# Optimization experiments

Measured on AMD Instinct MI355X. Metric: run time of the kernel, lower is better.

Reference implementation:

```python
import jax, jax.numpy as jnp
import numpy as np

N_USER, N_ITEM = 100000, 50000
D, H, B, E = 64, 64, 16384, 2000000

def _xavier(key, shape):
    fan_in, fan_out = shape[0], shape[1]
    lim = float(np.sqrt(6.0 / (fan_in + fan_out)))
    return jax.random.uniform(key, shape, jnp.float32, -lim, lim)

def setup_inputs() -> dict:
    key = jax.random.key(0)
    ks = jax.random.split(key, 16)
    inp = {
        "user_table": _xavier(ks[0], (N_USER, D)),
        "item_table": _xavier(ks[1], (N_ITEM, D)),
        "Wu": _xavier(ks[2], (D, D)),   # GCN_user weight ([in,out])
        "bu": jnp.zeros((D,), jnp.float32),
        "Wi": _xavier(ks[3], (D, D)),   # GCN_item weight
        "bi": jnp.zeros((D,), jnp.float32),
        "W1": _xavier(ks[4], (4 * D, 2 * H)),
        "b1": jnp.zeros((2 * H,), jnp.float32),
        "W2": _xavier(ks[5], (2 * H, H)),
        "b2": jnp.zeros((H,), jnp.float32),
        "W3": _xavier(ks[6], (H, 1)),
        "b3": jnp.zeros((1,), jnp.float32),
        "user_bias": jnp.zeros((N_USER, 1), jnp.float32),
        "item_bias": jnp.zeros((N_ITEM, 1), jnp.float32),
        "user_id": jax.random.randint(ks[7], (B,), 0, N_USER),
        "item_id": jax.random.randint(ks[8], (B,), 0, N_ITEM),
        "edge_user": jax.random.randint(ks[9], (E,), 0, N_USER),
        "edge_item": jax.random.randint(ks[10], (E,), 0, N_ITEM),
    }
    return inp

def reference(user_table, item_table, Wu, bu, Wi, bi, W1, b1, W2, b2, W3, b3,
              user_bias, item_bias, user_id, item_id, edge_user, edge_item):
    # sparse.mm(edge_ui, item_h)[user_id]: aggregate item embeddings per user
    agg_i = jax.ops.segment_sum(item_table[edge_item], edge_user, num_segments=N_USER)[user_id]
    agg_u = jax.ops.segment_sum(user_table[edge_user], edge_item, num_segments=N_ITEM)[item_id]
    ones_e = jnp.ones((edge_user.shape[0],), jnp.float32)
    deg_u = jax.ops.segment_sum(ones_e, edge_user, num_segments=N_USER)[user_id] + 1.0  # item_din
    deg_i = jax.ops.segment_sum(ones_e, edge_item, num_segments=N_ITEM)[item_id] + 1.0  # user_din
    gcn_item_h = agg_i / deg_u[:, None]   # [B, D]
    gcn_user_h = agg_u / deg_i[:, None]   # [B, D]
    # dropout p=0.3 is identity in eval mode
    gcn_user_out = jax.nn.relu(gcn_user_h @ Wu + bu)
    gcn_item_out = jax.nn.relu(gcn_item_h @ Wi + bi)
    u_emb = user_table[user_id]
    i_emb = item_table[item_id]
    x = jnp.concatenate([u_emb * i_emb,
                         u_emb * gcn_item_out,
                         gcn_user_out * i_emb,
                         gcn_user_out * gcn_item_out], axis=-1)  # [B, 4D]
    x1 = jnp.tanh(x @ W1 + b1)
    x2 = jnp.tanh(x1 @ W2 + b2)
    x3 = (x2 @ W3 + b3).reshape(-1)
    return x3 + user_bias[user_id, 0] + item_bias[item_id, 0]
```

## Files before the change

### kernel.cpp

```cpp
#include <hip/hip_runtime.h>
#include <cstdint>
#include <cstddef>

#define D 64
#define CAPU 96
#define CAPI 128
#define OCAP 4096

__global__ __launch_bounds__(256) void k_build_maps(const int* __restrict__ user_id,
                                                    const int* __restrict__ item_id,
                                                    int* __restrict__ map_u,
                                                    int* __restrict__ map_i, int B)
{
    int i = blockIdx.x * blockDim.x + threadIdx.x;
    if (i < B) {
        atomicCAS(&map_u[user_id[i]], -1, i);
        atomicCAS(&map_i[item_id[i]], -1, i);
    }
}

__global__ __launch_bounds__(256) void k_scatter(const int* __restrict__ edge_user,
                                                 const int* __restrict__ edge_item,
                                                 const int* __restrict__ map_u,
                                                 const int* __restrict__ map_i,
                                                 int* __restrict__ cntU,
                                                 int* __restrict__ cntI,
                                                 uint32_t* __restrict__ listU,
                                                 uint32_t* __restrict__ listI,
                                                 int* __restrict__ ovfCnt,
                                                 uint32_t* __restrict__ ovf, int E)
{
    int t = blockIdx.x * blockDim.x + threadIdx.x;
    int base = t * 4;
    if (base >= E) return;

    int us[4], is[4];
    int cnt4 = 4;
    if (base + 3 < E) {
        int4 eu = *(const int4*)(edge_user + base);
        int4 ei = *(const int4*)(edge_item + base);
        us[0] = eu.x; us[1] = eu.y; us[2] = eu.z; us[3] = eu.w;
        is[0] = ei.x; is[1] = ei.y; is[2] = ei.z; is[3] = ei.w;
    } else {
        cnt4 = E - base;
        for (int q = 0; q < cnt4; ++q) { us[q] = edge_user[base + q]; is[q] = edge_item[base + q]; }
    }

    #pragma unroll
    for (int q = 0; q < 4; ++q) {
        if (q >= cnt4) break;
        int u = us[q], it = is[q];
        int su = map_u[u];
        int si = map_i[it];
        if (su >= 0) {
            int pos = atomicAdd(&cntU[su * 16], 1);
            if (pos < CAPU) listU[(size_t)su * CAPU + pos] = (uint32_t)it;
            else { int o = atomicAdd(ovfCnt, 1);
                   if (o < OCAP) ovf[o] = ((uint32_t)su << 17) | (uint32_t)it; }
        }
        if (si >= 0) {
            int pos = atomicAdd(&cntI[si * 16], 1);
            if (pos < CAPI) listI[(size_t)si * CAPI + pos] = (uint32_t)u;
            else { int o = atomicAdd(ovfCnt, 1);
                   if (o < OCAP) ovf[o] = 0x80000000u | ((uint32_t)si << 17) | (uint32_t)u; }
        }
    }
}

__global__ __launch_bounds__(256) void k_gather(const uint32_t* __restrict__ listU,
                                                const uint32_t* __restrict__ listI,
                                                const int* __restrict__ cntU,
                                                const int* __restrict__ cntI,
                                                const float* __restrict__ user_table,
                                                const float* __restrict__ item_table,
                                                const int* __restrict__ ovfCnt,
                                                const uint32_t* __restrict__ ovf,
                                                float* __restrict__ aggIU,
                                                float* __restrict__ aggUI,
                                                int* __restrict__ degU,
                                                int* __restrict__ degI, int B)
{
    int gg = (blockIdx.x * blockDim.x + threadIdx.x) >> 4;
    if (gg >= 2 * B) return;
    int l16 = threadIdx.x & 15;
    int side = gg >= B;
    int slot = side ? gg - B : gg;

    int cnt = side ? cntI[slot * 16] : cntU[slot * 16];
    int caps = side ? CAPI : CAPU;
    int n = cnt < caps ? cnt : caps;
    const uint32_t* list = side ? (listI + (size_t)slot * CAPI)
                                : (listU + (size_t)slot * CAPU);
    const float4* table4 = (const float4*)(side ? user_table : item_table);

    float4 a0 = {0.f, 0.f, 0.f, 0.f};
    float4 a1 = {0.f, 0.f, 0.f, 0.f};
    int j = 0;
    #pragma unroll 2
    for (; j + 2 <= n; j += 2) {
        int r0 = (int)list[j];
        int r1 = (int)list[j + 1];
        float4 v0 = table4[(size_t)r0 * 16 + l16];
        float4 v1 = table4[(size_t)r1 * 16 + l16];
        a0.x += v0.x; a0.y += v0.y; a0.z += v0.z; a0.w += v0.w;
        a1.x += v1.x; a1.y += v1.y; a1.z += v1.z; a1.w += v1.w;
    }
    if (j < n) {
        int r0 = (int)list[j];
        float4 v0 = table4[(size_t)r0 * 16 + l16];
        a0.x += v0.x; a0.y += v0.y; a0.z += v0.z; a0.w += v0.w;
    }
    if (cnt > caps) {
        int on = *ovfCnt; if (on > OCAP) on = OCAP;
        for (int k = 0; k < on; ++k) {
            uint32_t p = ovf[k];
            if ((int)(p >> 31) == side && (int)((p >> 17) & 0x3FFFu) == slot) {
                float4 v = table4[(size_t)(p & 0x1FFFFu) * 16 + l16];
                a0.x += v.x; a0.y += v.y; a0.z += v.z; a0.w += v.w;
            }
        }
    }
    float4 acc = {a0.x + a1.x, a0.y + a1.y, a0.z + a1.z, a0.w + a1.w};
    float4* agg4 = (float4*)(side ? aggUI : aggIU);
    agg4[(size_t)slot * 16 + l16] = acc;
    if (l16 == 0) (side ? degI : degU)[slot] = cnt;
}

__global__ __launch_bounds__(1024) void k_build_x(const int* __restrict__ user_id,
                                                  const int* __restrict__ item_id,
                                                  const int* __restrict__ map_u,
                                                  const int* __restrict__ map_i,
                                                  const int* __restrict__ degU,
                                                  const int* __restrict__ degI,
                                                  const float* __restrict__ aggIU,
                                                  const float* __restrict__ aggUI,
                                                  const float* __restrict__ user_table,
                                                  const float* __restrict__ item_table,
                                                  const float* __restrict__ Wu,
                                                  const float* __restrict__ bu,
                                                  const float* __restrict__ Wi,
                                                  const float* __restrict__ bi,
                                                  float* __restrict__ x, int B)
{
    __shared__ float WuL[D * D];
    __shared__ float WiL[D * D];
    for (int t = threadIdx.x; t < D * D; t += blockDim.x) {
        WuL[t] = Wu[t];
        WiL[t] = Wi[t];
    }
    __syncthreads();

    int wid = (blockIdx.x * blockDim.x + threadIdx.x) >> 6;
    int lane = threadIdx.x & 63;
    if (wid >= B) return;

    int u  = user_id[wid];
    int it = item_id[wid];
    int su = map_u[u];
    int si = map_i[it];
    float du = (float)degU[su] + 1.0f;
    float di = (float)degI[si] + 1.0f;
    float gih = aggIU[(size_t)su * D + lane] / du;
    float guh = aggUI[(size_t)si * D + lane] / di;

    float accU = bu[lane];
    float accI = bi[lane];
    #pragma unroll 8
    for (int k = 0; k < D; ++k) {
        float gk = __shfl(guh, k);
        accU = fmaf(gk, WuL[k * D + lane], accU);
        float hk = __shfl(gih, k);
        accI = fmaf(hk, WiL[k * D + lane], accI);
    }
    float guo = fmaxf(accU, 0.0f);
    float gio = fmaxf(accI, 0.0f);
    float ue = user_table[(size_t)u * D + lane];
    float ie = item_table[(size_t)it * D + lane];

    size_t xb = (size_t)wid * 256;
    x[xb + lane]       = ue * ie;
    x[xb + 64 + lane]  = ue * gio;
    x[xb + 128 + lane] = guo * ie;
    x[xb + 192 + lane] = guo * gio;
}

__global__ __launch_bounds__(256) void k_gemm1(const float* __restrict__ x,
                                               const float* __restrict__ W1,
                                               const float* __restrict__ b1,
                                               float* __restrict__ x1, int B)
{
    __shared__ float xs[32][65];
    __shared__ float ws[32][128];
    int tid = threadIdx.x;
    int tx = tid & 31;
    int ty = tid >> 5;
    int row0 = blockIdx.x * 64;
    float acc[8][4] = {};

    for (int k0 = 0; k0 < 256; k0 += 32) {
        {
            int r = tid >> 2;
            int kk = (tid & 3) * 8;
            const float4* src = (const float4*)&x[(size_t)(row0 + r) * 256 + k0 + kk];
            float4 v0 = src[0], v1 = src[1];
            xs[kk + 0][r] = v0.x; xs[kk + 1][r] = v0.y; xs[kk + 2][r] = v0.z; xs[kk + 3][r] = v0.w;
            xs[kk + 4][r] = v1.x; xs[kk + 5][r] = v1.y; xs[kk + 6][r] = v1.z; xs[kk + 7][r] = v1.w;
        }
        {
            const float4* src = (const float4*)(W1 + (size_t)k0 * 128);
            float4* dst = (float4*)&ws[0][0];
            #pragma unroll
            for (int q = 0; q < 4; ++q) dst[tid + q * 256] = src[tid + q * 256];
        }
        __syncthreads();
        #pragma unroll
        for (int k = 0; k < 32; ++k) {
            float a[8], b[4];
            #pragma unroll
            for (int r = 0; r < 8; ++r) a[r] = xs[k][ty * 8 + r];
            #pragma unroll
            for (int c = 0; c < 4; ++c) b[c] = ws[k][tx + 32 * c];
            #pragma unroll
            for (int r = 0; r < 8; ++r)
                #pragma unroll
                for (int c = 0; c < 4; ++c)
                    acc[r][c] = fmaf(a[r], b[c], acc[r][c]);
        }
        __syncthreads();
    }
    #pragma unroll
    for (int r = 0; r < 8; ++r) {
        int row = row0 + ty * 8 + r;
        #pragma unroll
        for (int c = 0; c < 4; ++c) {
            int col = tx + 32 * c;
            x1[(size_t)row * 128 + col] = tanhf(acc[r][c] + b1[col]);
        }
    }
}

__global__ __launch_bounds__(256) void k_gemm2f(const float* __restrict__ x1,
                                                const float* __restrict__ W2,
                                                const float* __restrict__ b2,
                                                const float* __restrict__ W3,
                                                const float* __restrict__ b3,
                                                const float* __restrict__ user_bias,
                                                const float* __restrict__ item_bias,
                                                const int* __restrict__ user_id,
                                                const int* __restrict__ item_id,
                                                float* __restrict__ out, int B)
{
    __shared__ float xs[32][65];
    __shared__ float ws[32][64];
    int tid = threadIdx.x;
    int tx = tid & 15;
    int ty = tid >> 4;
    int row0 = blockIdx.x * 64;
    float acc[4][4] = {};

    for (int k0 = 0; k0 < 128; k0 += 32) {
        {
            int r = tid >> 2;
            int kk = (tid & 3) * 8;
            const float4* src = (const float4*)&x1[(size_t)(row0 + r) * 128 + k0 + kk];
            float4 v0 = src[0], v1 = src[1];
            xs[kk + 0][r] = v0.x; xs[kk + 1][r] = v0.y; xs[kk + 2][r] = v0.z; xs[kk + 3][r] = v0.w;
            xs[kk + 4][r] = v1.x; xs[kk + 5][r] = v1.y; xs[kk + 6][r] = v1.z; xs[kk + 7][r] = v1.w;
        }
        {
            const float4* src = (const float4*)(W2 + (size_t)k0 * 64);
            float4* dst = (float4*)&ws[0][0];
            #pragma unroll
            for (int q = 0; q < 2; ++q) dst[tid + q * 256] = src[tid + q * 256];
        }
        __syncthreads();
        #pragma unroll
        for (int k = 0; k < 32; ++k) {
            float a[4], b[4];
            #pragma unroll
            for (int r = 0; r < 4; ++r) a[r] = xs[k][ty * 4 + r];
            #pragma unroll
            for (int c = 0; c < 4; ++c) b[c] = ws[k][tx + 16 * c];
            #pragma unroll
            for (int r = 0; r < 4; ++r)
                #pragma unroll
                for (int c = 0; c < 4; ++c)
                    acc[r][c] = fmaf(a[r], b[c], acc[r][c]);
        }
        __syncthreads();
    }

    float w3v[4], b2v[4];
    #pragma unroll
    for (int c = 0; c < 4; ++c) {
        int col = tx + 16 * c;
        w3v[c] = W3[col];
        b2v[c] = b2[col];
    }
    #pragma unroll
    for (int r = 0; r < 4; ++r) {
        float p = 0.f;
        #pragma unroll
        for (int c = 0; c < 4; ++c)
            p += tanhf(acc[r][c] + b2v[c]) * w3v[c];
        p += __shfl_xor(p, 1);
        p += __shfl_xor(p, 2);
        p += __shfl_xor(p, 4);
        p += __shfl_xor(p, 8);
        if (tx == 0) {
            int row = row0 + ty * 4 + r;
            out[row] = p + b3[0] + user_bias[user_id[row]] + item_bias[item_id[row]];
        }
    }
}

extern "C" void kernel_launch(void* const* d_in, const int* in_sizes, int n_in,
                              void* d_out, int out_size, void* d_ws, size_t ws_size,
                              hipStream_t stream)
{
    const float* user_table = (const float*)d_in[0];
    const float* item_table = (const float*)d_in[1];
    const float* Wu = (const float*)d_in[2];
    const float* bu = (const float*)d_in[3];
    const float* Wi = (const float*)d_in[4];
    const float* bi = (const float*)d_in[5];
    const float* W1 = (const float*)d_in[6];
    const float* b1 = (const float*)d_in[7];
    const float* W2 = (const float*)d_in[8];
    const float* b2 = (const float*)d_in[9];
    const float* W3 = (const float*)d_in[10];
    const float* b3 = (const float*)d_in[11];
    const float* user_bias = (const float*)d_in[12];
    const float* item_bias = (const float*)d_in[13];
    const int* user_id = (const int*)d_in[14];
    const int* item_id = (const int*)d_in[15];
    const int* edge_user = (const int*)d_in[16];
    const int* edge_item = (const int*)d_in[17];

    const int N_USER = in_sizes[0] / D;
    const int N_ITEM = in_sizes[1] / D;
    const int B = in_sizes[14];
    const int E = in_sizes[16];

    char* ws = (char*)d_ws;
    const size_t aggIU_off = 0;
    const size_t aggUI_off = aggIU_off + (size_t)B * D * 4;
    const size_t degU_off  = aggUI_off + (size_t)B * D * 4;
    const size_t degI_off  = degU_off + (size_t)B * 4;
    const size_t mapu_off  = degI_off + (size_t)B * 4;
    const size_t mapi_off  = mapu_off + (size_t)N_USER * 4;
    size_t x_off = mapi_off + (size_t)N_ITEM * 4;
    x_off = (x_off + 255) & ~(size_t)255;
    const size_t x1_off = x_off + (size_t)B * 256 * 4;

    float* aggIU = (float*)(ws + aggIU_off);
    float* aggUI = (float*)(ws + aggUI_off);
    int*   degU  = (int*)(ws + degU_off);
    int*   degI  = (int*)(ws + degI_off);
    int*   map_u = (int*)(ws + mapu_off);
    int*   map_i = (int*)(ws + mapi_off);
    float* x  = (float*)(ws + x_off);
    float* x1 = (float*)(ws + x1_off);

    uint32_t* listU = (uint32_t*)(ws + x_off);
    uint32_t* listI = listU + (size_t)B * CAPU;
    int* cntU = (int*)(ws + x1_off);
    int* cntI = cntU + (size_t)B * 16;
    int* ovfCnt = cntI + (size_t)B * 16;
    uint32_t* ovf = (uint32_t*)(ovfCnt + 64);

    hipMemsetAsync(ws + mapu_off, 0xFF, (size_t)(N_USER + N_ITEM) * 4, stream);
    hipMemsetAsync(cntU, 0, (size_t)B * 16 * 4 * 2 + 256 + OCAP * 4, stream);

    k_build_maps<<<(B + 255) / 256, 256, 0, stream>>>(user_id, item_id, map_u, map_i, B);

    k_scatter<<<(E / 4 + 255) / 256, 256, 0, stream>>>(edge_user, edge_item, map_u, map_i,
                                                       cntU, cntI, listU, listI, ovfCnt, ovf, E);

    k_gather<<<(2 * B) / 16, 256, 0, stream>>>(listU, listI, cntU, cntI,
                                               user_table, item_table, ovfCnt, ovf,
                                               aggIU, aggUI, degU, degI, B);

    k_build_x<<<B / 16, 1024, 0, stream>>>(user_id, item_id, map_u, map_i, degU, degI,
                                           aggIU, aggUI, user_table, item_table,
                                           Wu, bu, Wi, bi, x, B);

    k_gemm1<<<B / 64, 256, 0, stream>>>(x, W1, b1, x1, B);

    k_gemm2f<<<B / 64, 256, 0, stream>>>(x1, W2, b2, W3, b3, user_bias, item_bias,
                                         user_id, item_id, (float*)d_out, B);
}
```

Baseline: 272.7 us.

## Fuse feature construction with MLP layers and tile GCN linear layers

The degree normalization moves into the gather kernel. The per-row shuffle GCN matmul is replaced by a tiled 32-row GEMM kernel that writes GCN outputs. The separate x-build, GEMM1 and GEMM2 kernels are merged into one MLP kernel that builds the elementwise products on the fly in shared memory, so the 16 MB x tensor and the x1 intermediate no longer round-trip through global memory. The cost is a heavier kernel with about 50 KB of shared memory, smaller 32-row tiles (fewer reuses of W1 per load), and the embedding rows being re-gathered per chunk.

```diff
diff --git a/kernel.cpp b/kernel.cpp
--- a/kernel.cpp
+++ b/kernel.cpp
@@ -6,6 +6,7 @@
 #define CAPU 96
 #define CAPI 128
 #define OCAP 4096
+#define GR 32
 
 __global__ __launch_bounds__(256) void k_build_maps(const int* __restrict__ user_id,
                                                     const int* __restrict__ item_id,
@@ -76,9 +77,7 @@
                                                 const int* __restrict__ ovfCnt,
                                                 const uint32_t* __restrict__ ovf,
                                                 float* __restrict__ aggIU,
-                                                float* __restrict__ aggUI,
-                                                int* __restrict__ degU,
-                                                int* __restrict__ degI, int B)
+                                                float* __restrict__ aggUI, int B)
 {
     int gg = (blockIdx.x * blockDim.x + threadIdx.x) >> 4;
     if (gg >= 2 * B) return;
@@ -120,197 +119,195 @@
             }
         }
     }
-    float4 acc = {a0.x + a1.x, a0.y + a1.y, a0.z + a1.z, a0.w + a1.w};
+    float inv = 1.0f / ((float)cnt + 1.0f);
+    float4 acc = {(a0.x + a1.x) * inv, (a0.y + a1.y) * inv,
+                  (a0.z + a1.z) * inv, (a0.w + a1.w) * inv};
     float4* agg4 = (float4*)(side ? aggUI : aggIU);
     agg4[(size_t)slot * 16 + l16] = acc;
-    if (l16 == 0) (side ? degI : degU)[slot] = cnt;
-}
-
-__global__ __launch_bounds__(1024) void k_build_x(const int* __restrict__ user_id,
-                                                  const int* __restrict__ item_id,
-                                                  const int* __restrict__ map_u,
-                                                  const int* __restrict__ map_i,
-                                                  const int* __restrict__ degU,
-                                                  const int* __restrict__ degI,
-                                                  const float* __restrict__ aggIU,
-                                                  const float* __restrict__ aggUI,
-                                                  const float* __restrict__ user_table,
-                                                  const float* __restrict__ item_table,
-                                                  const float* __restrict__ Wu,
-                                                  const float* __restrict__ bu,
-                                                  const float* __restrict__ Wi,
-                                                  const float* __restrict__ bi,
-                                                  float* __restrict__ x, int B)
-{
-    __shared__ float WuL[D * D];
-    __shared__ float WiL[D * D];
-    for (int t = threadIdx.x; t < D * D; t += blockDim.x) {
-        WuL[t] = Wu[t];
-        WiL[t] = Wi[t];
+}
+
+__global__ __launch_bounds__(256) void k_gcn(const int* __restrict__ user_id,
+                                             const int* __restrict__ item_id,
+                                             const int* __restrict__ map_u,
+                                             const int* __restrict__ map_i,
+                                             const float* __restrict__ aggIU,
+                                             const float* __restrict__ aggUI,
+                                             const float* __restrict__ Wi,
+                                             const float* __restrict__ bi,
+                                             const float* __restrict__ Wu,
+                                             const float* __restrict__ bu,
+                                             float* __restrict__ Xgi,
+                                             float* __restrict__ Xgu, int B)
+{
+    __shared__ float A[GR][68];
+    __shared__ float Wl[64][64];
+    __shared__ int sslot[GR];
+    int t = threadIdx.x;
+    int nb = B / GR;
+    int b = blockIdx.x;
+    int side = b >= nb;
+    int row0 = (side ? b - nb : b) * GR;
+
+    if (t < GR) {
+        int r = row0 + t;
+        sslot[t] = side ? map_i[item_id[r]] : map_u[user_id[r]];
+    }
+    {
+        const float4* Wg = (const float4*)(side ? Wu : Wi);
+        float4* Wl4 = (float4*)&Wl[0][0];
+        #pragma unroll
+        for (int q = 0; q < 4; ++q) Wl4[t + q * 256] = Wg[t + q * 256];
     }
     __syncthreads();
-
-    int wid = (blockIdx.x * blockDim.x + threadIdx.x) >> 6;
-    int lane = threadIdx.x & 63;
-    if (wid >= B) return;
-
-    int u  = user_id[wid];
-    int it = item_id[wid];
-    int su = map_u[u];
-    int si = map_i[it];
-    float du = (float)degU[su] + 1.0f;
-    float di = (float)degI[si] + 1.0f;
-    float gih = aggIU[(size_t)su * D + lane] / du;
-    float guh = aggUI[(size_t)si * D + lane] / di;
-
-    float accU = bu[lane];
-    float accI = bi[lane];
-    #pragma unroll 8
-    for (int k = 0; k < D; ++k) {
-        float gk = __shfl(guh, k);
-        accU = fmaf(gk, WuL[k * D + lane], accU);
-        float hk = __shfl(gih, k);
-        accI = fmaf(hk, WiL[k * D + lane], accI);
-    }
-    float guo = fmaxf(accU, 0.0f);
-    float gio = fmaxf(accI, 0.0f);
-    float ue = user_table[(size_t)u * D + lane];
-    float ie = item_table[(size_t)it * D + lane];
-
-    size_t xb = (size_t)wid * 256;
-    x[xb + lane]       = ue * ie;
-    x[xb + 64 + lane]  = ue * gio;
-    x[xb + 128 + lane] = guo * ie;
-    x[xb + 192 + lane] = guo * gio;
-}
-
-__global__ __launch_bounds__(256) void k_gemm1(const float* __restrict__ x,
-                                               const float* __restrict__ W1,
-                                               const float* __restrict__ b1,
-                                               float* __restrict__ x1, int B)
-{
-    __shared__ float xs[32][65];
-    __shared__ float ws[32][128];
-    int tid = threadIdx.x;
-    int tx = tid & 31;
-    int ty = tid >> 5;
-    int row0 = blockIdx.x * 64;
-    float acc[8][4] = {};
-
-    for (int k0 = 0; k0 < 256; k0 += 32) {
+    {
+        const float4* agg4 = (const float4*)(side ? aggUI : aggIU);
+        #pragma unroll
+        for (int q = 0; q < 2; ++q) {
+            int idx = t * 2 + q;
+            int r = idx >> 4, l16 = idx & 15;
+            ((float4*)&A[r][0])[l16] = agg4[(size_t)sslot[r] * 16 + l16];
+        }
+    }
+    __syncthreads();
+
+    const float* bias = side ? bu : bi;
+    int tx = t & 15, ty = t >> 4;
+    float acc[2][4] = {};
+    for (int k = 0; k < 64; ++k) {
+        float a0 = A[2 * ty][k];
+        float a1 = A[2 * ty + 1][k];
+        #pragma unroll
+        for (int c = 0; c < 4; ++c) {
+            float w = Wl[k][tx + 16 * c];
+            acc[0][c] = fmaf(a0, w, acc[0][c]);
+            acc[1][c] = fmaf(a1, w, acc[1][c]);
+        }
+    }
+    float* Xg = side ? Xgu : Xgi;
+    #pragma unroll
+    for (int r = 0; r < 2; ++r) {
+        int row = row0 + 2 * ty + r;
+        #pragma unroll
+        for (int c = 0; c < 4; ++c) {
+            int col = tx + 16 * c;
+            Xg[(size_t)row * 64 + col] = fmaxf(acc[r][c] + bias[col], 0.f);
+        }
+    }
+}
+
+__global__ __launch_bounds__(256) void k_mlp(const int* __restrict__ user_id,
+                                             const int* __restrict__ item_id,
+                                             const float* __restrict__ user_table,
+                                             const float* __restrict__ item_table,
+                                             const float* __restrict__ Xgi,
+                                             const float* __restrict__ Xgu,
+                                             const float* __restrict__ W1,
+                                             const float* __restrict__ b1,
+                                             const float* __restrict__ W2,
+                                             const float* __restrict__ b2,
+                                             const float* __restrict__ W3,
+                                             const float* __restrict__ b3,
+                                             const float* __restrict__ user_bias,
+                                             const float* __restrict__ item_bias,
+                                             float* __restrict__ out, int B)
+{
+    __shared__ float Fbuf[64][68];
+    __shared__ float WB[8192];
+    __shared__ int sU[GR], sI[GR];
+    int t = threadIdx.x;
+    int row0 = blockIdx.x * GR;
+    if (t < GR) { sU[t] = user_id[row0 + t]; sI[t] = item_id[row0 + t]; }
+    __syncthreads();
+
+    int tx1 = t & 31, ty1 = t >> 5;
+    float acc1[4][4] = {};
+
+    const int fkA[4] = {0, 0, 3, 3};
+    const int fkB[4] = {1, 2, 1, 2};
+    for (int j = 0; j < 4; ++j) {
+        #pragma unroll
+        for (int half = 0; half < 2; ++half) {
+            int kind = half ? fkB[j] : fkA[j];
+            #pragma unroll
+            for (int q = 0; q < 2; ++q) {
+                int idx = t * 2 + q;
+                int r = idx >> 4, l16 = idx & 15;
+                const float4* src;
+                size_t rowidx;
+                if (kind == 0)      { src = (const float4*)user_table; rowidx = (size_t)sU[r]; }
+                else if (kind == 1) { src = (const float4*)item_table; rowidx = (size_t)sI[r]; }
+                else if (kind == 2) { src = (const float4*)Xgi; rowidx = (size_t)(row0 + r); }
+                else                { src = (const float4*)Xgu; rowidx = (size_t)(row0 + r); }
+                ((float4*)&Fbuf[half * 32 + r][0])[l16] = src[rowidx * 16 + l16];
+            }
+        }
         {
-            int r = tid >> 2;
-            int kk = (tid & 3) * 8;
-            const float4* src = (const float4*)&x[(size_t)(row0 + r) * 256 + k0 + kk];
-            float4 v0 = src[0], v1 = src[1];
-            xs[kk + 0][r] = v0.x; xs[kk + 1][r] = v0.y; xs[kk + 2][r] = v0.z; xs[kk + 3][r] = v0.w;
-            xs[kk + 4][r] = v1.x; xs[kk + 5][r] = v1.y; xs[kk + 6][r] = v1.z; xs[kk + 7][r] = v1.w;
-        }
-        {
-            const float4* src = (const float4*)(W1 + (size_t)k0 * 128);
-            float4* dst = (float4*)&ws[0][0];
-            #pragma unroll
-            for (int q = 0; q < 4; ++q) dst[tid + q * 256] = src[tid + q * 256];
+            const float4* w4 = (const float4*)W1 + (size_t)j * 2048;
+            float4* d = (float4*)WB;
+            #pragma unroll
+            for (int q = 0; q < 8; ++q) d[t + q * 256] = w4[t + q * 256];
         }
         __syncthreads();
-        #pragma unroll
-        for (int k = 0; k < 32; ++k) {
-            float a[8], b[4];
-            #pragma unroll
-            for (int r = 0; r < 8; ++r) a[r] = xs[k][ty * 8 + r];
-            #pragma unroll
-            for (int c = 0; c < 4; ++c) b[c] = ws[k][tx + 32 * c];
-            #pragma unroll
-            for (int r = 0; r < 8; ++r)
-                #pragma unroll
-                for (int c = 0; c < 4; ++c)
-                    acc[r][c] = fmaf(a[r], b[c], acc[r][c]);
-        }
-        __syncthreads();
-    }
-    #pragma unroll
-    for (int r = 0; r < 8; ++r) {
-        int row = row0 + ty * 8 + r;
-        #pragma unroll
-        for (int c = 0; c < 4; ++c) {
-            int col = tx + 32 * c;
-            x1[(size_t)row * 128 + col] = tanhf(acc[r][c] + b1[col]);
-        }
-    }
-}
-
-__global__ __launch_bounds__(256) void k_gemm2f(const float* __restrict__ x1,
-                                                const float* __restrict__ W2,
-                                                const float* __restrict__ b2,
-                                                const float* __restrict__ W3,
-                                                const float* __restrict__ b3,
-                                                const float* __restrict__ user_bias,
-                                                const float* __restrict__ item_bias,
-                                                const int* __restrict__ user_id,
-                                                const int* __restrict__ item_id,
-                                                float* __restrict__ out, int B)
-{
-    __shared__ float xs[32][65];
-    __shared__ float ws[32][64];
-    int tid = threadIdx.x;
-    int tx = tid & 15;
-    int ty = tid >> 4;
-    int row0 = blockIdx.x * 64;
-    float acc[4][4] = {};
-
-    for (int k0 = 0; k0 < 128; k0 += 32) {
-        {
-            int r = tid >> 2;
-            int kk = (tid & 3) * 8;
-            const float4* src = (const float4*)&x1[(size_t)(row0 + r) * 128 + k0 + kk];
-            float4 v0 = src[0], v1 = src[1];
-            xs[kk + 0][r] = v0.x; xs[kk + 1][r] = v0.y; xs[kk + 2][r] = v0.z; xs[kk + 3][r] = v0.w;
-            xs[kk + 4][r] = v1.x; xs[kk + 5][r] = v1.y; xs[kk + 6][r] = v1.z; xs[kk + 7][r] = v1.w;
-        }
-        {
-            const float4* src = (const float4*)(W2 + (size_t)k0 * 64);
-            float4* dst = (float4*)&ws[0][0];
-            #pragma unroll
-            for (int q = 0; q < 2; ++q) dst[tid + q * 256] = src[tid + q * 256];
-        }
-        __syncthreads();
-        #pragma unroll
-        for (int k = 0; k < 32; ++k) {
+        for (int k = 0; k < 64; ++k) {
             float a[4], b[4];
             #pragma unroll
-            for (int r = 0; r < 4; ++r) a[r] = xs[k][ty * 4 + r];
-            #pragma unroll
-            for (int c = 0; c < 4; ++c) b[c] = ws[k][tx + 16 * c];
+            for (int r = 0; r < 4; ++r)
+                a[r] = Fbuf[4 * ty1 + r][k] * Fbuf[32 + 4 * ty1 + r][k];
+            #pragma unroll
+            for (int c = 0; c < 4; ++c) b[c] = WB[k * 128 + tx1 + 32 * c];
             #pragma unroll
             for (int r = 0; r < 4; ++r)
                 #pragma unroll
                 for (int c = 0; c < 4; ++c)
-                    acc[r][c] = fmaf(a[r], b[c], acc[r][c]);
+                    acc1[r][c] = fmaf(a[r], b[c], acc1[r][c]);
         }
         __syncthreads();
     }
 
-    float w3v[4], b2v[4];
+    float* x1t = &Fbuf[0][0];
     #pragma unroll
-    for (int c = 0; c < 4; ++c) {
-        int col = tx + 16 * c;
-        w3v[c] = W3[col];
-        b2v[c] = b2[col];
-    }
+    for (int r = 0; r < 4; ++r)
+        #pragma unroll
+        for (int c = 0; c < 4; ++c) {
+            int col = tx1 + 32 * c;
+            x1t[(4 * ty1 + r) * 132 + col] = tanhf(acc1[r][c] + b1[col]);
+        }
+    {
+        const float4* w4 = (const float4*)W2;
+        float4* d = (float4*)WB;
+        #pragma unroll
+        for (int q = 0; q < 8; ++q) d[t + q * 256] = w4[t + q * 256];
+    }
+    __syncthreads();
+
+    int tx2 = t & 15, ty2 = t >> 4;
+    float acc2[2][4] = {};
+    for (int k = 0; k < 128; ++k) {
+        float a0 = x1t[(2 * ty2) * 132 + k];
+        float a1 = x1t[(2 * ty2 + 1) * 132 + k];
+        #pragma unroll
+        for (int c = 0; c < 4; ++c) {
+            float w = WB[k * 64 + tx2 + 16 * c];
+            acc2[0][c] = fmaf(a0, w, acc2[0][c]);
+            acc2[1][c] = fmaf(a1, w, acc2[1][c]);
+        }
+    }
+    float b3v = b3[0];
     #pragma unroll
-    for (int r = 0; r < 4; ++r) {
+    for (int r = 0; r < 2; ++r) {
+        int lr = 2 * ty2 + r;
         float p = 0.f;
         #pragma unroll
-        for (int c = 0; c < 4; ++c)
-            p += tanhf(acc[r][c] + b2v[c]) * w3v[c];
+        for (int c = 0; c < 4; ++c) {
+            int col = tx2 + 16 * c;
+            p += tanhf(acc2[r][c] + b2[col]) * W3[col];
+        }
         p += __shfl_xor(p, 1);
         p += __shfl_xor(p, 2);
         p += __shfl_xor(p, 4);
         p += __shfl_xor(p, 8);
-        if (tx == 0) {
-            int row = row0 + ty * 4 + r;
-            out[row] = p + b3[0] + user_bias[user_id[row]] + item_bias[item_id[row]];
-        }
+        if (tx2 == 0)
+            out[row0 + lr] = p + b3v + user_bias[sU[lr]] + item_bias[sI[lr]];
     }
 }
 
@@ -343,34 +340,33 @@
     const int E = in_sizes[16];
 
     char* ws = (char*)d_ws;
-    const size_t aggIU_off = 0;
-    const size_t aggUI_off = aggIU_off + (size_t)B * D * 4;
-    const size_t degU_off  = aggUI_off + (size_t)B * D * 4;
-    const size_t degI_off  = degU_off + (size_t)B * 4;
-    const size_t mapu_off  = degI_off + (size_t)B * 4;
-    const size_t mapi_off  = mapu_off + (size_t)N_USER * 4;
-    size_t x_off = mapi_off + (size_t)N_ITEM * 4;
-    x_off = (x_off + 255) & ~(size_t)255;
-    const size_t x1_off = x_off + (size_t)B * 256 * 4;
+    size_t off = 0;
+    const size_t aggIU_off = off; off += (size_t)B * D * 4;
+    const size_t aggUI_off = off; off += (size_t)B * D * 4;
+    const size_t mapu_off  = off; off += (size_t)N_USER * 4;
+    const size_t mapi_off  = off; off += (size_t)N_ITEM * 4;
+    const size_t cntU_off  = off; off += (size_t)B * 16 * 4;
+    const size_t cntI_off  = off; off += (size_t)B * 16 * 4;
+    const size_t ovfc_off  = off; off += 256;
+    const size_t ovf_off   = off; off += (size_t)OCAP * 4;
+    const size_t listU_off = off; off += (size_t)B * CAPU * 4;
+    const size_t listI_off = off; off += (size_t)B * CAPI * 4;
 
     float* aggIU = (float*)(ws + aggIU_off);
     float* aggUI = (float*)(ws + aggUI_off);
-    int*   degU  = (int*)(ws + degU_off);
-    int*   degI  = (int*)(ws + degI_off);
     int*   map_u = (int*)(ws + mapu_off);
     int*   map_i = (int*)(ws + mapi_off);
-    float* x  = (float*)(ws + x_off);
-    float* x1 = (float*)(ws + x1_off);
-
-    uint32_t* listU = (uint32_t*)(ws + x_off);
-    uint32_t* listI = listU + (size_t)B * CAPU;
-    int* cntU = (int*)(ws + x1_off);
-    int* cntI = cntU + (size_t)B * 16;
-    int* ovfCnt = cntI + (size_t)B * 16;
-    uint32_t* ovf = (uint32_t*)(ovfCnt + 64);
+    int*   cntU  = (int*)(ws + cntU_off);
+    int*   cntI  = (int*)(ws + cntI_off);
+    int*   ovfCnt = (int*)(ws + ovfc_off);
+    uint32_t* ovf = (uint32_t*)(ws + ovf_off);
+    uint32_t* listU = (uint32_t*)(ws + listU_off);
+    uint32_t* listI = (uint32_t*)(ws + listI_off);
+    float* Xgi = (float*)(ws + listU_off);
+    float* Xgu = Xgi + (size_t)B * D;
 
     hipMemsetAsync(ws + mapu_off, 0xFF, (size_t)(N_USER + N_ITEM) * 4, stream);
-    hipMemsetAsync(cntU, 0, (size_t)B * 16 * 4 * 2 + 256 + OCAP * 4, stream);
+    hipMemsetAsync(ws + cntU_off, 0, (size_t)B * 16 * 4 * 2 + 256 + OCAP * 4, stream);
 
     k_build_maps<<<(B + 255) / 256, 256, 0, stream>>>(user_id, item_id, map_u, map_i, B);
 
@@ -379,14 +375,12 @@
 
     k_gather<<<(2 * B) / 16, 256, 0, stream>>>(listU, listI, cntU, cntI,
                                                user_table, item_table, ovfCnt, ovf,
-                                               aggIU, aggUI, degU, degI, B);
-
-    k_build_x<<<B / 16, 1024, 0, stream>>>(user_id, item_id, map_u, map_i, degU, degI,
-                                           aggIU, aggUI, user_table, item_table,
-                                           Wu, bu, Wi, bi, x, B);
-
-    k_gemm1<<<B / 64, 256, 0, stream>>>(x, W1, b1, x1, B);
-
-    k_gemm2f<<<B / 64, 256, 0, stream>>>(x1, W2, b2, W3, b3, user_bias, item_bias,
-                                         user_id, item_id, (float*)d_out, B);
-}
+                                               aggIU, aggUI, B);
+
+    k_gcn<<<2 * (B / GR), 256, 0, stream>>>(user_id, item_id, map_u, map_i,
+                                            aggIU, aggUI, Wi, bi, Wu, bu, Xgi, Xgu, B);
+
+    k_mlp<<<B / GR, 256, 0, stream>>>(user_id, item_id, user_table, item_table,
+                                      Xgi, Xgu, W1, b1, W2, b2, W3, b3,
+                                      user_bias, item_bias, (float*)d_out, B);
+}
```

Result: faster. 242.7 us (-11.0%).
